# Optimization experiments

Measured on AMD Instinct MI355X. Metric: run time of the kernel, lower is better.

## Reference

```python
import jax, jax.numpy as jnp
import numpy as np

B, L, D, H, O = 128, 256, 512, 1024, 2


def setup_inputs() -> dict:
    key = jax.random.key(0)
    ks = jax.random.split(key, 8)
    s = 1.0 / np.sqrt(H)
    sx = 1.0 / np.sqrt(D)
    return {
        "x": jax.random.normal(ks[0], (B, L, D), dtype=jnp.float32),
        "slen": jax.random.randint(ks[1], (B,), 0, L - 1),
        "Wh": jax.random.uniform(ks[2], (H, H), jnp.float32, -s, s),
        "bh": jax.random.uniform(ks[3], (H,), jnp.float32, -s, s),
        "Wx": jax.random.uniform(ks[4], (D, H), jnp.float32, -sx, sx),
        "bx": jax.random.uniform(ks[5], (H,), jnp.float32, -sx, sx),
        "Wo": jax.random.uniform(ks[6], (H, O), jnp.float32, -s, s),
        "bo": jax.random.uniform(ks[7], (O,), jnp.float32, -s, s),
    }


def reference(x, slen, Wh, bh, Wx, bx, Wo, bo):
    # x: (B, L, D) -> time-major (L, B, D)
    xT = jnp.transpose(x, (1, 0, 2))
    # input projection is time-independent: precompute Wx(x)+bx
    xp = xT @ Wx + bx  # (L, B, H)

    def step(carry, xpi):
        h, c = carry
        # All four 'gates' in the source share the same Wh/Wx, so a single
        # pre-activation z drives everything: i = f = o = sigmoid(z), g = tanh(z)
        z = h @ Wh + bh + xpi
        sg = jax.nn.sigmoid(z)
        g = jnp.tanh(z)
        c = sg * c + sg * g
        h = sg * jnp.tanh(c)
        return (h, c), h

    h0 = jnp.zeros((x.shape[0], Wh.shape[0]), dtype=x.dtype)
    _, hs = jax.lax.scan(step, (h0, h0), xp)  # (L, B, H)

    out = jax.nn.sigmoid(hs @ Wo + bo)  # (L, B, O)
    out = jnp.transpose(out, (1, 0, 2))  # (B, L, O)
    # positions il in [slen[b]+1, L) are overwritten with [0, 1]
    il = jnp.arange(out.shape[1])
    keep = (il[None, :] <= slen[:, None])[:, :, None]  # (B, L, 1)
    pad = jnp.array([0.0, 1.0], dtype=out.dtype)
    out = jnp.where(keep, out, pad)
    return out.reshape(-1, out.shape[-1])  # (B*L, O)
```

## Files before the change

kernel.cpp:

```cpp
#include <hip/hip_runtime.h>


#define B_ 128
#define L_ 256
#define D_ 512
#define H_ 1024

typedef __attribute__((ext_vector_type(8))) short short8;
typedef __attribute__((ext_vector_type(4))) float f32x4;
typedef __attribute__((ext_vector_type(2))) float f32x2;
typedef __attribute__((ext_vector_type(4))) unsigned short u16x4;
typedef __attribute__((ext_vector_type(4))) int i32x4;

__device__ __forceinline__ unsigned short f2bf(float f) {
    unsigned int u = __float_as_uint(f);
    return (unsigned short)((u + 0x8000u) >> 16);
}
__device__ __forceinline__ float bf2f(unsigned short s) {
    return __uint_as_float(((unsigned int)s) << 16);
}

__device__ __forceinline__ void st8(unsigned short* p, unsigned long long v) {
    __hip_atomic_store((unsigned long long*)p, v,
                       __ATOMIC_RELAXED, __HIP_MEMORY_SCOPE_AGENT);
}

template<int OFF>
__device__ __forceinline__ i32x4 ld16cc(const unsigned short* p) {
    i32x4 r;
    asm volatile("global_load_dwordx4 %0, %1, off offset:%2 sc0 sc1"
                 : "=v"(r) : "v"(p), "i"(OFF) : "memory");
    return r;
}
__device__ __forceinline__ void wait_vm0(i32x4& a, i32x4& b, i32x4& c, i32x4& d) {
    asm volatile("s_waitcnt vmcnt(0)" : "+v"(a), "+v"(b), "+v"(c), "+v"(d) :: "memory");
}
__device__ __forceinline__ void release_vm0() {
    asm volatile("s_waitcnt vmcnt(0)" ::: "memory");
}

__global__ __launch_bounds__(256) void k0_prep(
    const float* __restrict__ Wh, const float* __restrict__ Wx,
    const float* __restrict__ bh, const float* __restrict__ bx,
    unsigned short* __restrict__ Whb_t, unsigned short* __restrict__ Wxb_t,
    float* __restrict__ bxh, int* __restrict__ bar)
{
    const int stride = gridDim.x * blockDim.x;
    const int t0 = blockIdx.x * blockDim.x + threadIdx.x;
    for (int i = t0; i < H_ * H_; i += stride) {
        int n = i >> 10, k = i & 1023;
        Whb_t[i] = f2bf(Wh[k * H_ + n]);
    }
    for (int i = t0; i < H_ * D_; i += stride) {
        int n = i >> 9, k = i & 511;
        Wxb_t[i] = f2bf(Wx[k * H_ + n]);
    }
    for (int i = t0; i < H_; i += stride) bxh[i] = bx[i] + bh[i];
    for (int i = t0; i < 8 * 1024; i += stride) bar[i] = 0;
}

__global__ __launch_bounds__(256) void k1_xproj(
    const float* __restrict__ x, const unsigned short* __restrict__ Wxb_t,
    const float* __restrict__ bxh, unsigned short* __restrict__ xp)
{
    const int nt   = blockIdx.x & 3;
    const int mt   = blockIdx.x >> 2;
    const int w    = threadIdx.x >> 6;
    const int lane = threadIdx.x & 63;
    const int m    = lane & 15, q = lane >> 4;
    const int m0   = mt * 64;
    const int l    = m0 >> 7;
    const int brow = (m0 & 127) + w * 16;
    const int n0   = nt * 256;

    const float* ap = x + ((size_t)(brow + m) * L_ + l) * D_ + q * 8;

    f32x4 acc[16];
#pragma unroll
    for (int t = 0; t < 16; ++t) acc[t] = (f32x4){0.f, 0.f, 0.f, 0.f};

#pragma unroll 4
    for (int kk = 0; kk < 16; ++kk) {
        f32x4 av0 = *(const f32x4*)(ap + kk * 32);
        f32x4 av1 = *(const f32x4*)(ap + kk * 32 + 4);
        short8 a8;
        a8[0] = (short)f2bf(av0[0]); a8[1] = (short)f2bf(av0[1]);
        a8[2] = (short)f2bf(av0[2]); a8[3] = (short)f2bf(av0[3]);
        a8[4] = (short)f2bf(av1[0]); a8[5] = (short)f2bf(av1[1]);
        a8[6] = (short)f2bf(av1[2]); a8[7] = (short)f2bf(av1[3]);
#pragma unroll
        for (int t = 0; t < 16; ++t) {
            short8 b8 = *(const short8*)(Wxb_t +
                        (size_t)(n0 + t * 16 + m) * D_ + kk * 32 + q * 8);
            acc[t] = __builtin_amdgcn_mfma_f32_16x16x32_bf16(b8, a8, acc[t], 0, 0, 0);
        }
    }

#pragma unroll
    for (int t = 0; t < 16; ++t) {
        const int c0 = n0 + t * 16 + q * 4;
        f32x4 bias = *(const f32x4*)(bxh + c0);
        u16x4 o;
#pragma unroll
        for (int r = 0; r < 4; ++r) o[r] = f2bf(acc[t][r] + bias[r]);
        *(u16x4*)(xp + ((size_t)l * B_ + brow + m) * H_ + c0) = o;
    }
}

__global__ __launch_bounds__(256, 1) void k2_scan(
    const unsigned short* __restrict__ Whb_t,
    const unsigned short* __restrict__ xp,
    unsigned short* __restrict__ hs,
    int* __restrict__ bar)
{
    __shared__ unsigned short buf[2][16][1032];

    const int g    = blockIdx.x & 7;
    const int wg   = blockIdx.x >> 3;
    const int tid  = threadIdx.x;
    const int w    = tid >> 6;
    const int lane = tid & 63;
    const int mb   = lane & 15, q = lane >> 4;
    const int b0   = g * 16;
    const int colw = wg * 64 + w * 16;

    short8 afrag[32];
    {
        const unsigned short* wp = Whb_t + (size_t)(colw + mb) * H_ + q * 8;
#pragma unroll
        for (int kk = 0; kk < 32; ++kk)
            afrag[kk] = *(const short8*)(wp + kk * 32);
    }

    int* flags  = bar + g * 1024;
    int* myflag = flags + (wg * 4 + w) * 16;

    const int srow = tid >> 4;
    const int sci  = tid & 15;

    float c[4] = {0.f, 0.f, 0.f, 0.f};

    for (int l = 0; l < L_; ++l) {
        u16x4 xv = *(const u16x4*)(xp + ((size_t)l * B_ + b0 + mb) * H_ + colw + q * 4);

        unsigned short* lbuf = &buf[l & 1][0][0];
        if (l > 0) {
            while (true) {
                int f = __hip_atomic_load(flags + lane * 16,
                         __ATOMIC_RELAXED, __HIP_MEMORY_SCOPE_AGENT);
                if (__all(f >= l)) break;
                __builtin_amdgcn_s_sleep(2);
            }
            const unsigned short* gp =
                hs + ((size_t)(l - 1) * B_ + b0 + srow) * H_ + sci * 8;
            i32x4 v0, v1, v2, v3, v4, v5, v6, v7;
            v0 = ld16cc<0>(gp);    v1 = ld16cc<256>(gp);
            v2 = ld16cc<512>(gp);  v3 = ld16cc<768>(gp);
            v4 = ld16cc<1024>(gp); v5 = ld16cc<1280>(gp);
            v6 = ld16cc<1536>(gp); v7 = ld16cc<1792>(gp);
            wait_vm0(v0, v1, v2, v3);
            wait_vm0(v4, v5, v6, v7);
            unsigned short* lp = lbuf + srow * 1032 + sci * 8;
            *(i32x4*)(lp)        = v0;  *(i32x4*)(lp + 128)  = v1;
            *(i32x4*)(lp + 256)  = v2;  *(i32x4*)(lp + 384)  = v3;
            *(i32x4*)(lp + 512)  = v4;  *(i32x4*)(lp + 640)  = v5;
            *(i32x4*)(lp + 768)  = v6;  *(i32x4*)(lp + 896)  = v7;
        }
        __syncthreads();

        f32x4 acc0 = {0.f,0.f,0.f,0.f}, acc1 = {0.f,0.f,0.f,0.f};
        f32x4 acc2 = {0.f,0.f,0.f,0.f}, acc3 = {0.f,0.f,0.f,0.f};
        if (l > 0) {
            const unsigned short* rp = lbuf + mb * 1032 + q * 8;
#pragma unroll
            for (int kb = 0; kb < 32; kb += 4) {
                short8 bb0 = *(const short8*)(rp + (kb + 0) * 32);
                short8 bb1 = *(const short8*)(rp + (kb + 1) * 32);
                short8 bb2 = *(const short8*)(rp + (kb + 2) * 32);
                short8 bb3 = *(const short8*)(rp + (kb + 3) * 32);
                acc0 = __builtin_amdgcn_mfma_f32_16x16x32_bf16(afrag[kb + 0], bb0, acc0, 0, 0, 0);
                acc1 = __builtin_amdgcn_mfma_f32_16x16x32_bf16(afrag[kb + 1], bb1, acc1, 0, 0, 0);
                acc2 = __builtin_amdgcn_mfma_f32_16x16x32_bf16(afrag[kb + 2], bb2, acc2, 0, 0, 0);
                acc3 = __builtin_amdgcn_mfma_f32_16x16x32_bf16(afrag[kb + 3], bb3, acc3, 0, 0, 0);
            }
        }
        u16x4 o;
#pragma unroll
        for (int r = 0; r < 4; ++r) {
            float z  = acc0[r] + acc1[r] + acc2[r] + acc3[r] + bf2f(xv[r]);
            float e  = __expf(-z);
            float sg = 1.f / (1.f + e);
            float gg = 2.f / (1.f + e * e) - 1.f;
            c[r] = sg * (c[r] + gg);
            float ec = __expf(-2.f * c[r]);
            float th = 2.f / (1.f + ec) - 1.f;
            o[r] = f2bf(sg * th);
        }
        union { u16x4 v; unsigned long long u; } hu;
        hu.v = o;
        st8(hs + ((size_t)l * B_ + b0 + mb) * H_ + colw + q * 4, hu.u);
        release_vm0();
        if (lane == 0)
            __hip_atomic_store(myflag, l + 1,
                               __ATOMIC_RELAXED, __HIP_MEMORY_SCOPE_AGENT);
    }
}

__global__ __launch_bounds__(256) void k3_out(
    const unsigned short* __restrict__ hs,
    const float* __restrict__ Wo, const float* __restrict__ bo,
    const int* __restrict__ slen, float* __restrict__ out)
{
    const int w    = threadIdx.x >> 6;
    const int lane = threadIdx.x & 63;
    const int r    = blockIdx.x * 4 + w;
    const int b    = r >> 8;
    const int l    = r & 255;

    const unsigned short* hp = hs + ((size_t)l * B_ + b) * H_ + lane * 16;
    const float* wp = Wo + (size_t)lane * 32;
    float u0 = 0.f, u1 = 0.f;
#pragma unroll
    for (int j0 = 0; j0 < 16; j0 += 8) {
        short8 hv = *(const short8*)(hp + j0);
#pragma unroll
        for (int j = 0; j < 8; ++j) {
            float h = bf2f((unsigned short)hv[j]);
            f32x2 wv = *(const f32x2*)(wp + (j0 + j) * 2);
            u0 += h * wv[0];
            u1 += h * wv[1];
        }
    }
#pragma unroll
    for (int off = 32; off; off >>= 1) {
        u0 += __shfl_down(u0, off);
        u1 += __shfl_down(u1, off);
    }
    if (lane == 0) {
        float o0, o1;
        if (l <= slen[b]) {
            o0 = 1.f / (1.f + __expf(-(u0 + bo[0])));
            o1 = 1.f / (1.f + __expf(-(u1 + bo[1])));
        } else {
            o0 = 0.f; o1 = 1.f;
        }
        out[(size_t)r * 2]     = o0;
        out[(size_t)r * 2 + 1] = o1;
    }
}

extern "C" void kernel_launch(void* const* d_in, const int* in_sizes, int n_in,
                              void* d_out, int out_size, void* d_ws, size_t ws_size,
                              hipStream_t stream)
{
    const float* x    = (const float*)d_in[0];
    const int*   slen = (const int*)d_in[1];
    const float* Wh   = (const float*)d_in[2];
    const float* bh   = (const float*)d_in[3];
    const float* Wx   = (const float*)d_in[4];
    const float* bx   = (const float*)d_in[5];
    const float* Wo   = (const float*)d_in[6];
    const float* bo   = (const float*)d_in[7];
    float* out = (float*)d_out;

    char* ws = (char*)d_ws;
    unsigned short* Whb_t = (unsigned short*)(ws);
    unsigned short* Wxb_t = (unsigned short*)(ws + (2u << 20));
    float*          bxh   = (float*)(ws + (3u << 20));
    int*            bar   = (int*)(ws + (3u << 20) + 65536);
    unsigned short* xp    = (unsigned short*)(ws + (4u << 20));
    unsigned short* hs    = (unsigned short*)(ws + (68u << 20));

    k0_prep<<<512, 256, 0, stream>>>(Wh, Wx, bh, bx, Whb_t, Wxb_t, bxh, bar);
    k1_xproj<<<2048, 256, 0, stream>>>(x, Wxb_t, bxh, xp);
    k2_scan<<<128, 256, 0, stream>>>(Whb_t, xp, hs, bar);
    k3_out<<<8192, 256, 0, stream>>>(hs, Wo, bo, slen, out);
}
```

Baseline: 1.375 ms.

## Tile weight transpose through LDS, batch fragment loads, tighten scan spin-wait

The weight prep kernel now transposes Wh and Wx through a 64x65 shared-memory tile, so both global reads and writes are coalesced instead of strided. In the scan kernel the Wh fragment preload is issued as 32 back-to-back asm loads followed by a single wait. The spin loop no longer sleeps between flag polls, and the hidden-state copy into LDS begins storing the first half once it arrives. Busy polling without sleep may add memory traffic on the flag lines, and the prep grid changes to 385 blocks.

```diff
diff --git a/kernel.cpp b/kernel.cpp
--- a/kernel.cpp
+++ b/kernel.cpp
@@ -32,6 +32,9 @@
                  : "=v"(r) : "v"(p), "i"(OFF) : "memory");
     return r;
 }
+__device__ __forceinline__ void wait_vm4(i32x4& a, i32x4& b, i32x4& c, i32x4& d) {
+    asm volatile("s_waitcnt vmcnt(4)" : "+v"(a), "+v"(b), "+v"(c), "+v"(d) :: "memory");
+}
 __device__ __forceinline__ void wait_vm0(i32x4& a, i32x4& b, i32x4& c, i32x4& d) {
     asm volatile("s_waitcnt vmcnt(0)" : "+v"(a), "+v"(b), "+v"(c), "+v"(d) :: "memory");
 }
@@ -45,18 +48,42 @@
     unsigned short* __restrict__ Whb_t, unsigned short* __restrict__ Wxb_t,
     float* __restrict__ bxh, int* __restrict__ bar)
 {
-    const int stride = gridDim.x * blockDim.x;
-    const int t0 = blockIdx.x * blockDim.x + threadIdx.x;
-    for (int i = t0; i < H_ * H_; i += stride) {
-        int n = i >> 10, k = i & 1023;
-        Whb_t[i] = f2bf(Wh[k * H_ + n]);
-    }
-    for (int i = t0; i < H_ * D_; i += stride) {
-        int n = i >> 9, k = i & 511;
-        Wxb_t[i] = f2bf(Wx[k * H_ + n]);
-    }
-    for (int i = t0; i < H_; i += stride) bxh[i] = bx[i] + bh[i];
-    for (int i = t0; i < 8 * 1024; i += stride) bar[i] = 0;
+    __shared__ float tile[64][65];
+    const int blk = blockIdx.x;
+    const int t   = threadIdx.x;
+    const int c   = t & 63, r0 = t >> 6;
+
+    if (blk < 256) {
+        const int tk = (blk >> 4) * 64, tn = (blk & 15) * 64;
+#pragma unroll
+        for (int i = 0; i < 16; ++i) {
+            int r = i * 4 + r0;
+            tile[r][c] = Wh[(size_t)(tk + r) * H_ + tn + c];
+        }
+        __syncthreads();
+#pragma unroll
+        for (int i = 0; i < 16; ++i) {
+            int r = i * 4 + r0;
+            Whb_t[(size_t)(tn + r) * H_ + tk + c] = f2bf(tile[c][r]);
+        }
+    } else if (blk < 384) {
+        const int bi = blk - 256;
+        const int tk = (bi >> 4) * 64, tn = (bi & 15) * 64;
+#pragma unroll
+        for (int i = 0; i < 16; ++i) {
+            int r = i * 4 + r0;
+            tile[r][c] = Wx[(size_t)(tk + r) * H_ + tn + c];
+        }
+        __syncthreads();
+#pragma unroll
+        for (int i = 0; i < 16; ++i) {
+            int r = i * 4 + r0;
+            Wxb_t[(size_t)(tn + r) * D_ + tk + c] = f2bf(tile[c][r]);
+        }
+    } else {
+        for (int i = t; i < H_; i += 256) bxh[i] = bx[i] + bh[i];
+        for (int i = t; i < 8 * 1024; i += 256) bar[i] = 0;
+    }
 }
 
 __global__ __launch_bounds__(256) void k1_xproj(
@@ -129,7 +156,12 @@
         const unsigned short* wp = Whb_t + (size_t)(colw + mb) * H_ + q * 8;
 #pragma unroll
         for (int kk = 0; kk < 32; ++kk)
-            afrag[kk] = *(const short8*)(wp + kk * 32);
+            asm volatile("global_load_dwordx4 %0, %1, off offset:%2"
+                         : "=v"(afrag[kk]) : "v"(wp), "i"(kk * 64));
+        asm volatile("s_waitcnt vmcnt(0)" ::: "memory");
+#pragma unroll
+        for (int kk = 0; kk < 32; ++kk)
+            asm volatile("" : "+v"(afrag[kk]));
     }
 
     int* flags  = bar + g * 1024;
@@ -149,7 +181,6 @@
                 int f = __hip_atomic_load(flags + lane * 16,
                          __ATOMIC_RELAXED, __HIP_MEMORY_SCOPE_AGENT);
                 if (__all(f >= l)) break;
-                __builtin_amdgcn_s_sleep(2);
             }
             const unsigned short* gp =
                 hs + ((size_t)(l - 1) * B_ + b0 + srow) * H_ + sci * 8;
@@ -158,11 +189,11 @@
             v2 = ld16cc<512>(gp);  v3 = ld16cc<768>(gp);
             v4 = ld16cc<1024>(gp); v5 = ld16cc<1280>(gp);
             v6 = ld16cc<1536>(gp); v7 = ld16cc<1792>(gp);
-            wait_vm0(v0, v1, v2, v3);
-            wait_vm0(v4, v5, v6, v7);
             unsigned short* lp = lbuf + srow * 1032 + sci * 8;
+            wait_vm4(v0, v1, v2, v3);
             *(i32x4*)(lp)        = v0;  *(i32x4*)(lp + 128)  = v1;
             *(i32x4*)(lp + 256)  = v2;  *(i32x4*)(lp + 384)  = v3;
+            wait_vm0(v4, v5, v6, v7);
             *(i32x4*)(lp + 512)  = v4;  *(i32x4*)(lp + 640)  = v5;
             *(i32x4*)(lp + 768)  = v6;  *(i32x4*)(lp + 896)  = v7;
         }
@@ -271,7 +302,7 @@
     unsigned short* xp    = (unsigned short*)(ws + (4u << 20));
     unsigned short* hs    = (unsigned short*)(ws + (68u << 20));
 
-    k0_prep<<<512, 256, 0, stream>>>(Wh, Wx, bh, bx, Whb_t, Wxb_t, bxh, bar);
+    k0_prep<<<385, 256, 0, stream>>>(Wh, Wx, bh, bx, Whb_t, Wxb_t, bxh, bar);
     k1_xproj<<<2048, 256, 0, stream>>>(x, Wxb_t, bxh, xp);
     k2_scan<<<128, 256, 0, stream>>>(Whb_t, xp, hs, bar);
     k3_out<<<8192, 256, 0, stream>>>(hs, Wo, bo, slen, out);
```

New measurement: 1.362 ms. Within noise of the previous version (-1.0%).
